# Optimization experiments

Measured on AMD Instinct MI355X. Metric: run time of the kernel, lower is better.

## Reference

```python
import jax, jax.numpy as jnp
import numpy as np

DECAY = 0.99
EPS = 1e-05


def setup_inputs() -> dict:
    key = jax.random.key(0)
    k1, k2 = jax.random.split(key)
    B, C, H, W = 64, 256, 32, 32
    n_embed = 1024
    inp = jax.random.normal(k1, (B, C, H, W), dtype=jnp.float32)
    embed = jax.random.normal(k2, (C, n_embed), dtype=jnp.float32)
    cluster_size = jnp.ones((n_embed,), dtype=jnp.float32)
    embed_avg = embed.copy()
    return {"input": inp, "embed": embed, "cluster_size": cluster_size, "embed_avg": embed_avg}


def reference(input, embed, cluster_size, embed_avg):
    n_embed = embed.shape[1]
    x = jnp.transpose(input, (0, 2, 3, 1))            # B,H,W,C
    flatten = x.reshape(-1, x.shape[-1])              # N,C
    dist = ((flatten ** 2).sum(1, keepdims=True)
            - 2.0 * flatten @ embed
            + (embed ** 2).sum(0, keepdims=True))     # N,n_embed
    embed_ind = jnp.argmin(dist, axis=1)              # N
    quantize = jnp.take(embed.T, embed_ind, axis=0).reshape(x.shape)  # B,H,W,C
    embed_ind_out = embed_ind.reshape(x.shape[:-1])   # B,H,W

    # EMA codebook update (training=True)
    onehot_sum = jnp.zeros((n_embed,), dtype=flatten.dtype).at[embed_ind].add(1.0)
    embed_sum = jax.ops.segment_sum(flatten, embed_ind, num_segments=n_embed).T  # C,n_embed
    cluster_size_new = cluster_size * DECAY + onehot_sum * (1.0 - DECAY)
    embed_avg_new = embed_avg * DECAY + embed_sum * (1.0 - DECAY)
    n = cluster_size_new.sum()
    cs = (cluster_size_new + EPS) / (n + n_embed * EPS) * n
    embed_new = embed_avg_new / cs[None, :]

    diff = jax.lax.stop_gradient(quantize) - x
    quantize_st = x + jax.lax.stop_gradient(quantize - x)   # straight-through
    quantize_out = jnp.transpose(quantize_st, (0, 3, 1, 2)) # B,C,H,W
    return quantize_out, diff, embed_ind_out, embed_new, cluster_size_new, embed_avg_new
```

## Files before the change

kernel.cpp:

```cpp
#include <hip/hip_runtime.h>
#include <cstddef>

static constexpr int OUT_DIFF = 16777216;
static constexpr int OUT_IDX  = 33554432;
static constexpr int OUT_ENEW = 33619968;
static constexpr int OUT_CSN  = 33882112;
static constexpr int OUT_EAVG = 33883136;

__device__ __forceinline__ void gll16(const float* g, float* l) {
  __builtin_amdgcn_global_load_lds((const __attribute__((address_space(1))) void*)g,
                                   (__attribute__((address_space(3))) void*)l, 16, 0, 0);
}

__global__ __launch_bounds__(256) void k_prep(const float* __restrict__ embed,
                                              float* __restrict__ embedT,
                                              float* __restrict__ esq,
                                              int* __restrict__ cnt) {
  const int wg = blockIdx.x;
  const int tid = threadIdx.x;
  if (wg < 64) {
    __shared__ float tt[64 * 65];
    const int k0 = (wg >> 2) * 64, c0 = (wg & 3) * 64;
#pragma unroll
    for (int r = 0; r < 4; ++r) {
      int i = tid + r * 256;
      int cc = i >> 4, kL = (i & 15) * 4;
      float4 v = *(const float4*)(embed + (size_t)(c0 + cc) * 1024 + k0 + kL);
      tt[(kL + 0) * 65 + cc] = v.x;
      tt[(kL + 1) * 65 + cc] = v.y;
      tt[(kL + 2) * 65 + cc] = v.z;
      tt[(kL + 3) * 65 + cc] = v.w;
    }
    __syncthreads();
#pragma unroll
    for (int r = 0; r < 4; ++r) {
      int i = tid + r * 256;
      int kk = i >> 4, cL = (i & 15) * 4;
      float4 o;
      o.x = tt[kk * 65 + cL + 0];
      o.y = tt[kk * 65 + cL + 1];
      o.z = tt[kk * 65 + cL + 2];
      o.w = tt[kk * 65 + cL + 3];
      *(float4*)(embedT + (size_t)(k0 + kk) * 256 + c0 + cL) = o;
    }
  } else if (wg < 68) {
    const int k = (wg - 64) * 256 + tid;
    {
#pragma clang fp contract(off)
      float s = 0.f;
#pragma unroll 1
      for (int c = 0; c < 256; ++c) { float u = embed[(size_t)c * 1024 + k]; s += u * u; }
      esq[k] = s;
    }
  } else {
    ((int4*)cnt)[tid] = make_int4(0, 0, 0, 0);
  }
}

__global__ __launch_bounds__(256) void k_flatten(const float* __restrict__ inp,
                                                 float* __restrict__ flat) {
  const int tid = threadIdx.x;
  const int b = blockIdx.x >> 4;
  const int hw0 = (blockIdx.x & 15) * 64;
  __shared__ float t[64 * 257];
#pragma unroll
  for (int r = 0; r < 16; ++r) {
    int i = tid + r * 256;
    int c = i >> 4, l = i & 15;
    float4 v = *(const float4*)(inp + (size_t)b * 262144 + (size_t)c * 1024 + hw0 + l * 4);
    t[(l * 4 + 0) * 257 + c] = v.x;
    t[(l * 4 + 1) * 257 + c] = v.y;
    t[(l * 4 + 2) * 257 + c] = v.z;
    t[(l * 4 + 3) * 257 + c] = v.w;
  }
  __syncthreads();
#pragma unroll
  for (int r = 0; r < 16; ++r) {
    int i = tid + r * 256;
    int hw = i >> 6, c4 = (i & 63) * 4;
    float4 o;
    o.x = t[hw * 257 + c4 + 0];
    o.y = t[hw * 257 + c4 + 1];
    o.z = t[hw * 257 + c4 + 2];
    o.w = t[hw * 257 + c4 + 3];
    *(float4*)(flat + ((size_t)(b * 1024 + hw0 + hw)) * 256 + c4) = o;
  }
}

__global__ __launch_bounds__(256) void k_argmin(const float* __restrict__ inp,
                                                const float* __restrict__ embed,
                                                const float* __restrict__ esq,
                                                int* __restrict__ idx_out,
                                                float* __restrict__ idxf_out,
                                                int* __restrict__ cnt) {
  __shared__ float xs[2][8][128];
  __shared__ float es[2][8][256];
  __shared__ float xsqh[2][128];
  __shared__ float xsq_s[128];

  const int tid = threadIdx.x;
  const int lane = tid & 63;
  const int w = tid >> 6;
  const int n0 = blockIdx.x * 128;
  const int b = n0 >> 10;
  const int hw0 = n0 & 1023;
  const float* xbase = inp + (size_t)b * 262144 + hw0;

  {
#pragma clang fp contract(off)
    const int p = tid & 127, h = tid >> 7;
    const float* xb = xbase + (size_t)(h * 128) * 1024 + p;
    float r[8];
#pragma unroll
    for (int j = 0; j < 8; ++j) { float v = xb[(size_t)j * 1024]; r[j] = v * v; }
#pragma unroll 1
    for (int blk = 1; blk < 16; ++blk) {
#pragma unroll
      for (int j = 0; j < 8; ++j) { float v = xb[(size_t)(blk * 8 + j) * 1024]; r[j] += v * v; }
    }
    xsqh[h][p] = ((r[0] + r[1]) + (r[2] + r[3])) + ((r[4] + r[5]) + (r[6] + r[7]));
    __syncthreads();
    if (tid < 128) xsq_s[tid] = xsqh[0][tid] + xsqh[1][tid];
  }

  const int tc = tid & 15, tr = tid >> 4;
  float bestv[8];
  int besti[8];
#pragma unroll
  for (int p = 0; p < 8; ++p) { bestv[p] = 3.0e38f; besti[p] = 0; }

#define STAGE(buf, c0)                                                               \
  do {                                                                               \
    gll16(xbase + (size_t)((c0) + 2 * w + (lane >> 5)) * 1024 + (lane & 31) * 4,     \
          &xs[buf][0][0] + w * 256);                                                 \
    gll16(embed + (size_t)((c0) + w) * 1024 + k0 + lane * 4,                         \
          &es[buf][0][0] + w * 256);                                                 \
    gll16(embed + (size_t)((c0) + 4 + w) * 1024 + k0 + lane * 4,                     \
          &es[buf][0][0] + (4 + w) * 256);                                           \
  } while (0)

#pragma unroll 1
  for (int kt = 0; kt < 4; ++kt) {
    const int k0 = kt * 256;
    float acc[8][16];
#pragma unroll
    for (int p = 0; p < 8; ++p)
#pragma unroll
      for (int j = 0; j < 16; ++j) acc[p][j] = 0.f;

    STAGE(0, 0);
    __syncthreads();

#pragma unroll 1
    for (int cs = 0; cs < 32; ++cs) {
      const int cur = cs & 1;
      if (cs < 31) STAGE(cur ^ 1, (cs + 1) * 8);
#pragma unroll
      for (int cc = 0; cc < 8; ++cc) {
        alignas(16) float xr[8];
        alignas(16) float er[16];
        *(float4*)&xr[0] = *(float4*)&xs[cur][cc][tr * 8];
        *(float4*)&xr[4] = *(float4*)&xs[cur][cc][tr * 8 + 4];
#pragma unroll
        for (int g = 0; g < 4; ++g)
          *(float4*)&er[g * 4] = *(float4*)&es[cur][cc][g * 64 + tc * 4];
#pragma unroll
        for (int p = 0; p < 8; ++p)
#pragma unroll
          for (int j = 0; j < 16; ++j)
            acc[p][j] = __builtin_fmaf(xr[p], er[j], acc[p][j]);
      }
      __syncthreads();
    }

    alignas(16) float esqr[16];
#pragma unroll
    for (int g = 0; g < 4; ++g)
      *(float4*)&esqr[g * 4] = *(const float4*)(esq + k0 + g * 64 + tc * 4);
#pragma unroll
    for (int p = 0; p < 8; ++p) {
      float xq = xsq_s[tr * 8 + p];
#pragma unroll
      for (int g = 0; g < 4; ++g)
#pragma unroll
        for (int jj = 0; jj < 4; ++jj) {
          int j = g * 4 + jj;
          float d = (xq - 2.0f * acc[p][j]) + esqr[j];
          int k = k0 + g * 64 + tc * 4 + jj;
          if (d < bestv[p]) { bestv[p] = d; besti[p] = k; }
        }
    }
  }
#undef STAGE

#pragma unroll
  for (int p = 0; p < 8; ++p) {
    float v = bestv[p];
    int ii = besti[p];
#pragma unroll
    for (int off = 1; off < 16; off <<= 1) {
      float ov = __shfl_xor(v, off);
      int oi = __shfl_xor(ii, off);
      if (ov < v || (ov == v && oi < ii)) { v = ov; ii = oi; }
    }
    if (tc == 0) {
      int n = n0 + tr * 8 + p;
      idx_out[n] = ii;
      idxf_out[n] = (float)ii;
      atomicAdd(cnt + ii, 1);
    }
  }
}

__global__ __launch_bounds__(1024) void k_scan(const int* __restrict__ cnt,
                                               const float* __restrict__ cs_in,
                                               int* __restrict__ offs,
                                               int* __restrict__ cursor,
                                               float* __restrict__ csn_out,
                                               float* __restrict__ nval) {
  __shared__ int sc[1024];
  __shared__ float red[1024];
  const int tid = threadIdx.x;
  const int c = cnt[tid];
  const float csv = cs_in[tid];
  sc[tid] = c;
  red[tid] = csv;
  __syncthreads();
#pragma unroll 1
  for (int off = 1; off < 1024; off <<= 1) {
    int v = sc[tid];
    int add = (tid >= off) ? sc[tid - off] : 0;
    __syncthreads();
    sc[tid] = v + add;
    __syncthreads();
  }
  const int incl = sc[tid];
  const int start = incl - c;
  offs[tid] = start;
  cursor[tid] = start;
  if (tid == 1023) offs[1024] = incl;
  csn_out[tid] = csv * 0.99f + (float)c * 0.01f;
#pragma unroll 1
  for (int off = 512; off > 0; off >>= 1) {
    if (tid < off) red[tid] += red[tid + off];
    __syncthreads();
  }
  if (tid == 0) nval[0] = 0.99f * red[0] + 0.01f * 65536.0f;
}

__global__ __launch_bounds__(256) void k_scatter(const int* __restrict__ idx,
                                                 int* __restrict__ cursor,
                                                 int* __restrict__ bucket) {
  const int n = blockIdx.x * 256 + threadIdx.x;
  const int k = idx[n];
  const int pos = atomicAdd(cursor + k, 1);
  bucket[pos] = n;
}

__global__ __launch_bounds__(256) void k_update(const int* __restrict__ offs,
                                                const int* __restrict__ bucket,
                                                const float* __restrict__ flat,
                                                float* __restrict__ sums) {
  const int k = blockIdx.x;
  const int tid = threadIdx.x;
  const int w = tid >> 6, lane = tid & 63;
  __shared__ float sums_s[4][256];
  const int start = offs[k], end = offs[k + 1];
  float4 acc = make_float4(0.f, 0.f, 0.f, 0.f);
#pragma unroll 1
  for (int e = start + w; e < end; e += 4) {
    const float* row = flat + (size_t)bucket[e] * 256;
    float4 x4 = *(const float4*)(row + lane * 4);
    acc.x += x4.x; acc.y += x4.y; acc.z += x4.z; acc.w += x4.w;
  }
  *(float4*)&sums_s[w][lane * 4] = acc;
  __syncthreads();
  const float s = ((sums_s[0][tid] + sums_s[1][tid]) + sums_s[2][tid]) + sums_s[3][tid];
  sums[(size_t)k * 256 + tid] = s;
}

__global__ __launch_bounds__(256) void k_ema(const float* __restrict__ sums,
                                             const float* __restrict__ eavg,
                                             const float* __restrict__ csn,
                                             const float* __restrict__ nval,
                                             float* __restrict__ eavgn,
                                             float* __restrict__ enew) {
  __shared__ float t[64 * 65];
  __shared__ float csks[64];
  const int tid = threadIdx.x;
  const int k0 = (blockIdx.x >> 2) * 64, c0 = (blockIdx.x & 3) * 64;
  if (tid < 64) {
    float nv = nval[0];
    float cv = csn[k0 + tid];
    csks[tid] = (cv + 1e-5f) / (nv + 0.01024f) * nv;
  }
#pragma unroll
  for (int r = 0; r < 4; ++r) {
    int i = tid + r * 256;
    int kk = i >> 4, cL = (i & 15) * 4;
    float4 v = *(const float4*)(sums + (size_t)(k0 + kk) * 256 + c0 + cL);
    t[(cL + 0) * 65 + kk] = v.x;
    t[(cL + 1) * 65 + kk] = v.y;
    t[(cL + 2) * 65 + kk] = v.z;
    t[(cL + 3) * 65 + kk] = v.w;
  }
  __syncthreads();
#pragma unroll
  for (int r = 0; r < 4; ++r) {
    int i = tid + r * 256;
    int c = i >> 4, kL = (i & 15) * 4;
    size_t o = (size_t)(c0 + c) * 1024 + k0 + kL;
    float4 ev = *(const float4*)(eavg + o);
    float4 ean, en;
    ean.x = ev.x * 0.99f + t[c * 65 + kL + 0] * 0.01f;
    ean.y = ev.y * 0.99f + t[c * 65 + kL + 1] * 0.01f;
    ean.z = ev.z * 0.99f + t[c * 65 + kL + 2] * 0.01f;
    ean.w = ev.w * 0.99f + t[c * 65 + kL + 3] * 0.01f;
    en.x = ean.x / csks[kL + 0];
    en.y = ean.y / csks[kL + 1];
    en.z = ean.z / csks[kL + 2];
    en.w = ean.w / csks[kL + 3];
    *(float4*)(eavgn + o) = ean;
    *(float4*)(enew + o) = en;
  }
}

__global__ __launch_bounds__(256) void k_diffq(const int* __restrict__ idx,
                                               const float* __restrict__ embedT,
                                               float* __restrict__ flat_diff,
                                               float* __restrict__ q_out) {
  const int tid = threadIdx.x;
  const int b = blockIdx.x >> 4;
  const int hw0 = (blockIdx.x & 15) * 64;
  const int n0 = b * 1024 + hw0;
  __shared__ float t[64 * 257];
#pragma unroll
  for (int r = 0; r < 16; ++r) {
    int i = tid + r * 256;
    int hw = i >> 6, c4 = (i & 63) * 4;
    int n = n0 + hw;
    int kk = idx[n];
    float4 q = *(const float4*)(embedT + (size_t)kk * 256 + c4);
    float4 x = *(const float4*)(flat_diff + (size_t)n * 256 + c4);
    float4 d;
    d.x = q.x - x.x; d.y = q.y - x.y; d.z = q.z - x.z; d.w = q.w - x.w;
    *(float4*)(flat_diff + (size_t)n * 256 + c4) = d;
    t[hw * 257 + c4 + 0] = x.x + d.x;
    t[hw * 257 + c4 + 1] = x.y + d.y;
    t[hw * 257 + c4 + 2] = x.z + d.z;
    t[hw * 257 + c4 + 3] = x.w + d.w;
  }
  __syncthreads();
#pragma unroll
  for (int r = 0; r < 16; ++r) {
    int i = tid + r * 256;
    int c = i >> 4, l = i & 15;
    float4 o;
    o.x = t[(l * 4 + 0) * 257 + c];
    o.y = t[(l * 4 + 1) * 257 + c];
    o.z = t[(l * 4 + 2) * 257 + c];
    o.w = t[(l * 4 + 3) * 257 + c];
    *(float4*)(q_out + (size_t)b * 262144 + (size_t)c * 1024 + hw0 + l * 4) = o;
  }
}

extern "C" void kernel_launch(void* const* d_in, const int* in_sizes, int n_in,
                              void* d_out, int out_size, void* d_ws, size_t ws_size,
                              hipStream_t stream) {
  (void)in_sizes; (void)n_in; (void)out_size; (void)ws_size;
  const float* inp   = (const float*)d_in[0];
  const float* embed = (const float*)d_in[1];
  const float* cs_in = (const float*)d_in[2];
  const float* eavg  = (const float*)d_in[3];
  float* out = (float*)d_out;

  int*   idx_ws = (int*)d_ws;
  int*   bucket = idx_ws + 65536;
  int*   cnt    = bucket + 65536;
  int*   offs   = cnt + 1024;
  int*   cursor = offs + 1536;
  float* wsf    = (float*)d_ws;
  float* nval   = wsf + 136192;
  float* esq    = wsf + 136448;
  float* sums   = wsf + 137472;
  float* embedT = wsf + 399616;

  float* flat = out + OUT_DIFF;

  hipLaunchKernelGGL(k_prep,    dim3(69),   dim3(256),  0, stream, embed, embedT, esq, cnt);
  hipLaunchKernelGGL(k_flatten, dim3(1024), dim3(256),  0, stream, inp, flat);
  hipLaunchKernelGGL(k_argmin,  dim3(512),  dim3(256),  0, stream, inp, embed, esq,
                     idx_ws, out + OUT_IDX, cnt);
  hipLaunchKernelGGL(k_scan,    dim3(1),    dim3(1024), 0, stream, cnt, cs_in, offs, cursor,
                     out + OUT_CSN, nval);
  hipLaunchKernelGGL(k_scatter, dim3(256),  dim3(256),  0, stream, idx_ws, cursor, bucket);
  hipLaunchKernelGGL(k_update,  dim3(1024), dim3(256),  0, stream, offs, bucket, flat, sums);
  hipLaunchKernelGGL(k_ema,     dim3(64),   dim3(256),  0, stream, sums, eavg, out + OUT_CSN,
                     nval, out + OUT_EAVG, out + OUT_ENEW);
  hipLaunchKernelGGL(k_diffq,   dim3(1024), dim3(256),  0, stream, idx_ws, embedT, flat, out);
}
```

Baseline: 1.093 ms.

## Drop flatten pass, compute segment sums from diff, and restructure argmin without LDS

Removes the separate flatten kernel: diffq now transposes the input itself and runs before the update kernel. The update kernel then reconstructs segment sums as count*code minus the summed diff rows, which saves one full pass over the activations. The argmin kernel is rewritten to 32 rows per block with each wavefront covering all 1024 codes, reading operands straight from global memory instead of double-buffered LDS staging. The risks are lower data reuse in the distance GEMM and a small change in float rounding of embed_sum.

```diff
diff --git a/kernel.cpp b/kernel.cpp
--- a/kernel.cpp
+++ b/kernel.cpp
@@ -6,11 +6,6 @@
 static constexpr int OUT_ENEW = 33619968;
 static constexpr int OUT_CSN  = 33882112;
 static constexpr int OUT_EAVG = 33883136;
-
-__device__ __forceinline__ void gll16(const float* g, float* l) {
-  __builtin_amdgcn_global_load_lds((const __attribute__((address_space(1))) void*)g,
-                                   (__attribute__((address_space(3))) void*)l, 16, 0, 0);
-}
 
 __global__ __launch_bounds__(256) void k_prep(const float* __restrict__ embed,
                                               float* __restrict__ embedT,
@@ -57,58 +52,26 @@
   }
 }
 
-__global__ __launch_bounds__(256) void k_flatten(const float* __restrict__ inp,
-                                                 float* __restrict__ flat) {
-  const int tid = threadIdx.x;
-  const int b = blockIdx.x >> 4;
-  const int hw0 = (blockIdx.x & 15) * 64;
-  __shared__ float t[64 * 257];
-#pragma unroll
-  for (int r = 0; r < 16; ++r) {
-    int i = tid + r * 256;
-    int c = i >> 4, l = i & 15;
-    float4 v = *(const float4*)(inp + (size_t)b * 262144 + (size_t)c * 1024 + hw0 + l * 4);
-    t[(l * 4 + 0) * 257 + c] = v.x;
-    t[(l * 4 + 1) * 257 + c] = v.y;
-    t[(l * 4 + 2) * 257 + c] = v.z;
-    t[(l * 4 + 3) * 257 + c] = v.w;
-  }
-  __syncthreads();
-#pragma unroll
-  for (int r = 0; r < 16; ++r) {
-    int i = tid + r * 256;
-    int hw = i >> 6, c4 = (i & 63) * 4;
-    float4 o;
-    o.x = t[hw * 257 + c4 + 0];
-    o.y = t[hw * 257 + c4 + 1];
-    o.z = t[hw * 257 + c4 + 2];
-    o.w = t[hw * 257 + c4 + 3];
-    *(float4*)(flat + ((size_t)(b * 1024 + hw0 + hw)) * 256 + c4) = o;
-  }
-}
-
 __global__ __launch_bounds__(256) void k_argmin(const float* __restrict__ inp,
                                                 const float* __restrict__ embed,
                                                 const float* __restrict__ esq,
                                                 int* __restrict__ idx_out,
                                                 float* __restrict__ idxf_out,
                                                 int* __restrict__ cnt) {
-  __shared__ float xs[2][8][128];
-  __shared__ float es[2][8][256];
-  __shared__ float xsqh[2][128];
-  __shared__ float xsq_s[128];
+  __shared__ float xsqh[64];
+  __shared__ float xsq_s[32];
 
   const int tid = threadIdx.x;
   const int lane = tid & 63;
   const int w = tid >> 6;
-  const int n0 = blockIdx.x * 128;
+  const int n0 = blockIdx.x * 32;
   const int b = n0 >> 10;
-  const int hw0 = n0 & 1023;
-  const float* xbase = inp + (size_t)b * 262144 + hw0;
-
-  {
+  const int hwb = n0 & 1023;
+  const float* xbase = inp + (size_t)b * 262144 + hwb;
+
+  if (tid < 64) {
 #pragma clang fp contract(off)
-    const int p = tid & 127, h = tid >> 7;
+    const int p = tid & 31, h = tid >> 5;
     const float* xb = xbase + (size_t)(h * 128) * 1024 + p;
     float r[8];
 #pragma unroll
@@ -118,93 +81,70 @@
 #pragma unroll
       for (int j = 0; j < 8; ++j) { float v = xb[(size_t)(blk * 8 + j) * 1024]; r[j] += v * v; }
     }
-    xsqh[h][p] = ((r[0] + r[1]) + (r[2] + r[3])) + ((r[4] + r[5]) + (r[6] + r[7]));
-    __syncthreads();
-    if (tid < 128) xsq_s[tid] = xsqh[0][tid] + xsqh[1][tid];
-  }
-
-  const int tc = tid & 15, tr = tid >> 4;
-  float bestv[8];
-  int besti[8];
-#pragma unroll
-  for (int p = 0; p < 8; ++p) { bestv[p] = 3.0e38f; besti[p] = 0; }
-
-#define STAGE(buf, c0)                                                               \
-  do {                                                                               \
-    gll16(xbase + (size_t)((c0) + 2 * w + (lane >> 5)) * 1024 + (lane & 31) * 4,     \
-          &xs[buf][0][0] + w * 256);                                                 \
-    gll16(embed + (size_t)((c0) + w) * 1024 + k0 + lane * 4,                         \
-          &es[buf][0][0] + w * 256);                                                 \
-    gll16(embed + (size_t)((c0) + 4 + w) * 1024 + k0 + lane * 4,                     \
-          &es[buf][0][0] + (4 + w) * 256);                                           \
-  } while (0)
-
-#pragma unroll 1
-  for (int kt = 0; kt < 4; ++kt) {
-    const int k0 = kt * 256;
-    float acc[8][16];
+    xsqh[h * 32 + p] = ((r[0] + r[1]) + (r[2] + r[3])) + ((r[4] + r[5]) + (r[6] + r[7]));
+  }
+  __syncthreads();
+  if (tid < 32) xsq_s[tid] = xsqh[tid] + xsqh[32 + tid];
+  __syncthreads();
+
+  const float* xptr = xbase + w * 8;
+  const float* eptr = embed + lane * 4;
+
+  float acc[8][16];
+#pragma unroll
+  for (int p = 0; p < 8; ++p)
+#pragma unroll
+    for (int j = 0; j < 16; ++j) acc[p][j] = 0.f;
+
+#pragma unroll 1
+  for (int c = 0; c < 256; ++c) {
+    const float* xc = xptr + (size_t)c * 1024;
+    const float* ec = eptr + (size_t)c * 1024;
+    float4 x0 = *(const float4*)(xc);
+    float4 x1 = *(const float4*)(xc + 4);
+    float4 e0 = *(const float4*)(ec);
+    float4 e1 = *(const float4*)(ec + 256);
+    float4 e2 = *(const float4*)(ec + 512);
+    float4 e3 = *(const float4*)(ec + 768);
+    float xr[8] = {x0.x, x0.y, x0.z, x0.w, x1.x, x1.y, x1.z, x1.w};
+    float er[16] = {e0.x, e0.y, e0.z, e0.w, e1.x, e1.y, e1.z, e1.w,
+                    e2.x, e2.y, e2.z, e2.w, e3.x, e3.y, e3.z, e3.w};
 #pragma unroll
     for (int p = 0; p < 8; ++p)
 #pragma unroll
-      for (int j = 0; j < 16; ++j) acc[p][j] = 0.f;
-
-    STAGE(0, 0);
-    __syncthreads();
-
-#pragma unroll 1
-    for (int cs = 0; cs < 32; ++cs) {
-      const int cur = cs & 1;
-      if (cs < 31) STAGE(cur ^ 1, (cs + 1) * 8);
-#pragma unroll
-      for (int cc = 0; cc < 8; ++cc) {
-        alignas(16) float xr[8];
-        alignas(16) float er[16];
-        *(float4*)&xr[0] = *(float4*)&xs[cur][cc][tr * 8];
-        *(float4*)&xr[4] = *(float4*)&xs[cur][cc][tr * 8 + 4];
-#pragma unroll
-        for (int g = 0; g < 4; ++g)
-          *(float4*)&er[g * 4] = *(float4*)&es[cur][cc][g * 64 + tc * 4];
-#pragma unroll
-        for (int p = 0; p < 8; ++p)
-#pragma unroll
-          for (int j = 0; j < 16; ++j)
-            acc[p][j] = __builtin_fmaf(xr[p], er[j], acc[p][j]);
+      for (int j = 0; j < 16; ++j)
+        acc[p][j] = __builtin_fmaf(xr[p], er[j], acc[p][j]);
+  }
+
+  float esqr[16];
+#pragma unroll
+  for (int g = 0; g < 4; ++g)
+    *(float4*)&esqr[g * 4] = *(const float4*)(esq + g * 256 + lane * 4);
+  float xq[8];
+#pragma unroll
+  for (int p = 0; p < 8; ++p) xq[p] = xsq_s[w * 8 + p];
+
+#pragma unroll 1
+  for (int p = 0; p < 8; ++p) {
+    float v = 3.0e38f;
+    int ii = 0;
+#pragma unroll
+    for (int g = 0; g < 4; ++g)
+#pragma unroll
+      for (int q = 0; q < 4; ++q) {
+        int j = g * 4 + q;
+        float d = (xq[p] - 2.0f * acc[p][j]) + esqr[j];
+        int k = g * 256 + lane * 4 + q;
+        if (d < v) { v = d; ii = k; }
       }
-      __syncthreads();
-    }
-
-    alignas(16) float esqr[16];
-#pragma unroll
-    for (int g = 0; g < 4; ++g)
-      *(float4*)&esqr[g * 4] = *(const float4*)(esq + k0 + g * 64 + tc * 4);
-#pragma unroll
-    for (int p = 0; p < 8; ++p) {
-      float xq = xsq_s[tr * 8 + p];
-#pragma unroll
-      for (int g = 0; g < 4; ++g)
-#pragma unroll
-        for (int jj = 0; jj < 4; ++jj) {
-          int j = g * 4 + jj;
-          float d = (xq - 2.0f * acc[p][j]) + esqr[j];
-          int k = k0 + g * 64 + tc * 4 + jj;
-          if (d < bestv[p]) { bestv[p] = d; besti[p] = k; }
-        }
-    }
-  }
-#undef STAGE
-
-#pragma unroll
-  for (int p = 0; p < 8; ++p) {
-    float v = bestv[p];
-    int ii = besti[p];
-#pragma unroll
-    for (int off = 1; off < 16; off <<= 1) {
+#pragma unroll
+    for (int off = 1; off < 64; off <<= 1) {
       float ov = __shfl_xor(v, off);
       int oi = __shfl_xor(ii, off);
       if (ov < v || (ov == v && oi < ii)) { v = ov; ii = oi; }
     }
-    if (tc == 0) {
-      int n = n0 + tr * 8 + p;
+    if (lane == 0) {
+      int n = n0 + w * 8 + p;
       idx_out[n] = ii;
       idxf_out[n] = (float)ii;
       atomicAdd(cnt + ii, 1);
@@ -257,9 +197,64 @@
   bucket[pos] = n;
 }
 
+__global__ __launch_bounds__(256) void k_diffq(const int* __restrict__ idx,
+                                               const float* __restrict__ embedT,
+                                               const float* __restrict__ inp,
+                                               float* __restrict__ diff,
+                                               float* __restrict__ q_out) {
+  const int tid = threadIdx.x;
+  const int b = blockIdx.x >> 4;
+  const int hw0 = (blockIdx.x & 15) * 64;
+  const int n0 = b * 1024 + hw0;
+  __shared__ float t[64 * 257];
+#pragma unroll
+  for (int r = 0; r < 16; ++r) {
+    int i = tid + r * 256;
+    int c = i >> 4, l = i & 15;
+    float4 v = *(const float4*)(inp + (size_t)b * 262144 + (size_t)c * 1024 + hw0 + l * 4);
+    t[(l * 4 + 0) * 257 + c] = v.x;
+    t[(l * 4 + 1) * 257 + c] = v.y;
+    t[(l * 4 + 2) * 257 + c] = v.z;
+    t[(l * 4 + 3) * 257 + c] = v.w;
+  }
+  __syncthreads();
+#pragma unroll
+  for (int r = 0; r < 16; ++r) {
+    int i = tid + r * 256;
+    int hw = i >> 6, c4 = (i & 63) * 4;
+    int n = n0 + hw;
+    int kk = idx[n];
+    float4 q = *(const float4*)(embedT + (size_t)kk * 256 + c4);
+    float x0 = t[hw * 257 + c4 + 0];
+    float x1 = t[hw * 257 + c4 + 1];
+    float x2 = t[hw * 257 + c4 + 2];
+    float x3 = t[hw * 257 + c4 + 3];
+    float4 d;
+    d.x = q.x - x0; d.y = q.y - x1; d.z = q.z - x2; d.w = q.w - x3;
+    *(float4*)(diff + (size_t)n * 256 + c4) = d;
+    t[hw * 257 + c4 + 0] = x0 + d.x;
+    t[hw * 257 + c4 + 1] = x1 + d.y;
+    t[hw * 257 + c4 + 2] = x2 + d.z;
+    t[hw * 257 + c4 + 3] = x3 + d.w;
+  }
+  __syncthreads();
+#pragma unroll
+  for (int r = 0; r < 16; ++r) {
+    int i = tid + r * 256;
+    int c = i >> 4, l = i & 15;
+    float4 o;
+    o.x = t[(l * 4 + 0) * 257 + c];
+    o.y = t[(l * 4 + 1) * 257 + c];
+    o.z = t[(l * 4 + 2) * 257 + c];
+    o.w = t[(l * 4 + 3) * 257 + c];
+    *(float4*)(q_out + (size_t)b * 262144 + (size_t)c * 1024 + hw0 + l * 4) = o;
+  }
+}
+
 __global__ __launch_bounds__(256) void k_update(const int* __restrict__ offs,
                                                 const int* __restrict__ bucket,
-                                                const float* __restrict__ flat,
+                                                const float* __restrict__ diff,
+                                                const float* __restrict__ embedT,
                                                 float* __restrict__ sums) {
   const int k = blockIdx.x;
   const int tid = threadIdx.x;
@@ -269,14 +264,15 @@
   float4 acc = make_float4(0.f, 0.f, 0.f, 0.f);
 #pragma unroll 1
   for (int e = start + w; e < end; e += 4) {
-    const float* row = flat + (size_t)bucket[e] * 256;
-    float4 x4 = *(const float4*)(row + lane * 4);
-    acc.x += x4.x; acc.y += x4.y; acc.z += x4.z; acc.w += x4.w;
+    const float* row = diff + (size_t)bucket[e] * 256;
+    float4 d4 = *(const float4*)(row + lane * 4);
+    acc.x += d4.x; acc.y += d4.y; acc.z += d4.z; acc.w += d4.w;
   }
   *(float4*)&sums_s[w][lane * 4] = acc;
   __syncthreads();
-  const float s = ((sums_s[0][tid] + sums_s[1][tid]) + sums_s[2][tid]) + sums_s[3][tid];
-  sums[(size_t)k * 256 + tid] = s;
+  const float dsum = ((sums_s[0][tid] + sums_s[1][tid]) + sums_s[2][tid]) + sums_s[3][tid];
+  const float cntf = (float)(end - start);
+  sums[(size_t)k * 256 + tid] = cntf * embedT[(size_t)k * 256 + tid] - dsum;
 }
 
 __global__ __launch_bounds__(256) void k_ema(const float* __restrict__ sums,
@@ -325,45 +321,6 @@
   }
 }
 
-__global__ __launch_bounds__(256) void k_diffq(const int* __restrict__ idx,
-                                               const float* __restrict__ embedT,
-                                               float* __restrict__ flat_diff,
-                                               float* __restrict__ q_out) {
-  const int tid = threadIdx.x;
-  const int b = blockIdx.x >> 4;
-  const int hw0 = (blockIdx.x & 15) * 64;
-  const int n0 = b * 1024 + hw0;
-  __shared__ float t[64 * 257];
-#pragma unroll
-  for (int r = 0; r < 16; ++r) {
-    int i = tid + r * 256;
-    int hw = i >> 6, c4 = (i & 63) * 4;
-    int n = n0 + hw;
-    int kk = idx[n];
-    float4 q = *(const float4*)(embedT + (size_t)kk * 256 + c4);
-    float4 x = *(const float4*)(flat_diff + (size_t)n * 256 + c4);
-    float4 d;
-    d.x = q.x - x.x; d.y = q.y - x.y; d.z = q.z - x.z; d.w = q.w - x.w;
-    *(float4*)(flat_diff + (size_t)n * 256 + c4) = d;
-    t[hw * 257 + c4 + 0] = x.x + d.x;
-    t[hw * 257 + c4 + 1] = x.y + d.y;
-    t[hw * 257 + c4 + 2] = x.z + d.z;
-    t[hw * 257 + c4 + 3] = x.w + d.w;
-  }
-  __syncthreads();
-#pragma unroll
-  for (int r = 0; r < 16; ++r) {
-    int i = tid + r * 256;
-    int c = i >> 4, l = i & 15;
-    float4 o;
-    o.x = t[(l * 4 + 0) * 257 + c];
-    o.y = t[(l * 4 + 1) * 257 + c];
-    o.z = t[(l * 4 + 2) * 257 + c];
-    o.w = t[(l * 4 + 3) * 257 + c];
-    *(float4*)(q_out + (size_t)b * 262144 + (size_t)c * 1024 + hw0 + l * 4) = o;
-  }
-}
-
 extern "C" void kernel_launch(void* const* d_in, const int* in_sizes, int n_in,
                               void* d_out, int out_size, void* d_ws, size_t ws_size,
                               hipStream_t stream) {
@@ -385,17 +342,16 @@
   float* sums   = wsf + 137472;
   float* embedT = wsf + 399616;
 
-  float* flat = out + OUT_DIFF;
-
   hipLaunchKernelGGL(k_prep,    dim3(69),   dim3(256),  0, stream, embed, embedT, esq, cnt);
-  hipLaunchKernelGGL(k_flatten, dim3(1024), dim3(256),  0, stream, inp, flat);
-  hipLaunchKernelGGL(k_argmin,  dim3(512),  dim3(256),  0, stream, inp, embed, esq,
+  hipLaunchKernelGGL(k_argmin,  dim3(2048), dim3(256),  0, stream, inp, embed, esq,
                      idx_ws, out + OUT_IDX, cnt);
   hipLaunchKernelGGL(k_scan,    dim3(1),    dim3(1024), 0, stream, cnt, cs_in, offs, cursor,
                      out + OUT_CSN, nval);
   hipLaunchKernelGGL(k_scatter, dim3(256),  dim3(256),  0, stream, idx_ws, cursor, bucket);
-  hipLaunchKernelGGL(k_update,  dim3(1024), dim3(256),  0, stream, offs, bucket, flat, sums);
+  hipLaunchKernelGGL(k_diffq,   dim3(1024), dim3(256),  0, stream, idx_ws, embedT, inp,
+                     out + OUT_DIFF, out);
+  hipLaunchKernelGGL(k_update,  dim3(1024), dim3(256),  0, stream, offs, bucket,
+                     out + OUT_DIFF, embedT, sums);
   hipLaunchKernelGGL(k_ema,     dim3(64),   dim3(256),  0, stream, sums, eavg, out + OUT_CSN,
                      nval, out + OUT_EAVG, out + OUT_ENEW);
-  hipLaunchKernelGGL(k_diffq,   dim3(1024), dim3(256),  0, stream, idx_ws, embedT, flat, out);
-}
+}
```

Result: slower. 1.168 ms (+6.8%).
